# Kernel tuning notes

Measured on AMD Instinct MI355X. Metric: run time of the kernel, lower is better.

Reference implementation:

```python
import jax, jax.numpy as jnp
import numpy as np

WS = (5, 8, 8)   # window_size (Wz, Wh, Ww)
SS = (2, 4, 4)   # shift_size  (Sz, Sh, Sw)
EPS = 1e-5


def _rel_pos_index(ws):
    Wz, Wh, Ww = ws
    coords = np.stack(np.meshgrid(np.arange(Wz), np.arange(Wh), np.arange(Ww), indexing='ij'))
    cf = coords.reshape(3, -1)                      # (3, N)
    rel = cf[:, :, None] - cf[:, None, :]           # (3, N, N)
    rel = rel.transpose(1, 2, 0).astype(np.int64)   # (N, N, 3)
    rel[..., 0] += Wz - 1
    rel[..., 1] += Wh - 1
    rel[..., 2] += Ww - 1
    rel[..., 0] *= (2 * Wh - 1) * (2 * Ww - 1)
    rel[..., 1] *= (2 * Ww - 1)
    return rel.sum(-1)                              # (N, N)


def _shift_mask(Z, H, W, ws, ss):
    Wz, Wh, Ww = ws
    Sz, Sh, Sw = ss
    img = np.zeros((Z, H, W), dtype=np.float32)
    cnt = 0
    for zs in (slice(0, -Wz), slice(-Wz, -Sz), slice(-Sz, None)):
        for hs in (slice(0, -Wh), slice(-Wh, -Sh), slice(-Sh, None)):
            for wl in (slice(0, -Ww), slice(-Ww, -Sw), slice(-Sw, None)):
                img[zs, hs, wl] = cnt
                cnt += 1
    mw = img.reshape(Z // Wz, Wz, H // Wh, Wh, W // Ww, Ww)
    mw = mw.transpose(0, 2, 4, 1, 3, 5).reshape(-1, Wz * Wh * Ww)  # (nW, N)
    diff = mw[:, None, :] - mw[:, :, None]                          # (nW, N, N)
    return np.where(diff != 0, np.float32(-100.0), np.float32(0.0))


def _layernorm(x, g, b):
    mu = jnp.mean(x, axis=-1, keepdims=True)
    var = jnp.var(x, axis=-1, keepdims=True)
    return (x - mu) * jax.lax.rsqrt(var + EPS) * g + b


def setup_inputs() -> dict:
    key = jax.random.key(0)
    ks = jax.random.split(key, 6)
    B, C, Z, H, W = 2, 192, 10, 48, 48
    nH = 6
    hidden = 4 * C
    tbl = (2 * WS[0] - 1) * (2 * WS[1] - 1) * (2 * WS[2] - 1)
    return {
        'x': jax.random.normal(ks[0], (B, C, Z, H, W), jnp.float32),
        'norm1_g': jnp.ones((C,), jnp.float32),
        'norm1_b': jnp.zeros((C,), jnp.float32),
        'qkv_w': jax.random.normal(ks[1], (3 * C, C), jnp.float32) * 0.02,
        'qkv_b': jnp.zeros((3 * C,), jnp.float32),
        'proj_w': jax.random.normal(ks[2], (C, C), jnp.float32) * 0.02,
        'proj_b': jnp.zeros((C,), jnp.float32),
        'rpb_table': jax.random.normal(ks[3], (tbl, nH), jnp.float32) * 0.02,
        'norm2_g': jnp.ones((C,), jnp.float32),
        'norm2_b': jnp.zeros((C,), jnp.float32),
        'fc1_w': jax.random.normal(ks[4], (hidden, C), jnp.float32) * 0.02,
        'fc1_b': jnp.zeros((hidden,), jnp.float32),
        'fc2_w': jax.random.normal(ks[5], (C, hidden), jnp.float32) * 0.02,
        'fc2_b': jnp.zeros((C,), jnp.float32),
    }


def reference(x, norm1_g, norm1_b, qkv_w, qkv_b, proj_w, proj_b, rpb_table,
              norm2_g, norm2_b, fc1_w, fc1_b, fc2_w, fc2_b):
    B, C, Z, H, W = x.shape
    Wz, Wh, Ww = WS
    Sz, Sh, Sw = SS
    nH = rpb_table.shape[1]
    hd = C // nH
    N = Wz * Wh * Ww
    scale = hd ** -0.5

    h = jnp.transpose(x, (0, 2, 3, 4, 1))            # (B,Z,H,W,C) channels-last
    shortcut = h
    h = _layernorm(h, norm1_g, norm1_b)
    # cyclic shift
    h = jnp.roll(h, shift=(-Sz, -Sh, -Sw), axis=(1, 2, 3))
    # window partition -> (BW, N, C)
    win = h.reshape(B, Z // Wz, Wz, H // Wh, Wh, W // Ww, Ww, C)
    win = win.transpose(0, 1, 3, 5, 2, 4, 6, 7).reshape(-1, N, C)
    BW = win.shape[0]

    qkv = win @ qkv_w.T + qkv_b                      # (BW, N, 3C)
    qkv = qkv.reshape(BW, N, 3, nH, hd)
    q = jnp.transpose(qkv[:, :, 0], (0, 2, 1, 3)) * scale   # (BW,nH,N,hd)
    k = jnp.transpose(qkv[:, :, 1], (0, 2, 1, 3))
    v = jnp.transpose(qkv[:, :, 2], (0, 2, 1, 3))

    attn = jnp.einsum('bhnd,bhmd->bhnm', q, k)       # (BW,nH,N,N)
    idx = _rel_pos_index(WS)                          # static (N,N)
    bias = rpb_table[idx.reshape(-1)].reshape(N, N, nH)
    attn = attn + jnp.transpose(bias, (2, 0, 1))[None]

    mask = jnp.asarray(_shift_mask(Z, H, W, WS, SS)) # (nW,N,N), static
    nW = mask.shape[0]
    attn = attn.reshape(B, nW, nH, N, N) + mask[None, :, None]
    attn = jax.nn.softmax(attn.reshape(BW, nH, N, N), axis=-1)

    out = jnp.einsum('bhnm,bhmd->bhnd', attn, v)     # (BW,nH,N,hd)
    out = jnp.transpose(out, (0, 2, 1, 3)).reshape(BW, N, C)
    out = out @ proj_w.T + proj_b

    # window reverse -> (B,Z,H,W,C)
    out = out.reshape(B, Z // Wz, H // Wh, W // Ww, Wz, Wh, Ww, C)
    out = out.transpose(0, 1, 4, 2, 5, 3, 6, 7).reshape(B, Z, H, W, C)
    out = jnp.roll(out, shift=(Sz, Sh, Sw), axis=(1, 2, 3))

    h = shortcut + out
    h2 = _layernorm(h, norm2_g, norm2_b)
    h2 = jax.nn.gelu(h2 @ fc1_w.T + fc1_b, approximate=False)
    h2 = h2 @ fc2_w.T + fc2_b
    h = h + h2
    return jnp.transpose(h, (0, 4, 1, 2, 3))          # back to (B,C,Z,H,W)
```

## Files before the change

### kernel.cpp

```cpp
#include <hip/hip_runtime.h>
#include <hip/hip_bf16.h>

typedef __hip_bfloat16 bf16;
typedef __attribute__((ext_vector_type(4))) float f32x4;
typedef __attribute__((ext_vector_type(8))) short bf16x8;
typedef __attribute__((ext_vector_type(4))) short bf16x4;
typedef __attribute__((ext_vector_type(4))) int i32x4;

#define DEVINL __device__ __forceinline__

constexpr int SPB = 23040;
constexpr int TOK = 46080;
constexpr int NWT = 320;
constexpr int NHEAD = 6;
constexpr int HD = 32;
constexpr int HID = 768;
constexpr int TBL = 2025;
constexpr float SCALE = 0.17677669529663687f;

DEVINL float b2f(bf16 v) { return __bfloat162float(v); }
DEVINL float bflo(unsigned u) { unsigned w = u << 16; return __builtin_bit_cast(float, w); }

DEVINL unsigned cvtpk(float a, float b) {
  unsigned r;
  asm("v_cvt_pk_bf16_f32 %0, %1, %2" : "=v"(r) : "v"(a), "v"(b));
  return r;
}

DEVINL f32x4 mfma16(bf16x4 a, bf16x4 b, f32x4 c) {
#if __has_builtin(__builtin_amdgcn_mfma_f32_16x16x16bf16_1k)
  return __builtin_amdgcn_mfma_f32_16x16x16bf16_1k(a, b, c, 0, 0, 0);
#elif __has_builtin(__builtin_amdgcn_mfma_f32_16x16x16_bf16)
  return __builtin_amdgcn_mfma_f32_16x16x16_bf16(a, b, c, 0, 0, 0);
#else
  f32x4 d;
  asm volatile("v_mfma_f32_16x16x16_bf16 %0, %1, %2, %3\n\ts_nop 7\n\ts_nop 7"
               : "=v"(d) : "v"(a), "v"(b), "v"(c));
  return d;
#endif
}

DEVINL void gload16(const bf16* g, bf16* l) {
  __builtin_amdgcn_global_load_lds(
      (const __attribute__((address_space(1))) void*)g,
      (__attribute__((address_space(3))) void*)l, 16, 0, 0);
}

__global__ void k_flag(const unsigned* __restrict__ g1, int* __restrict__ flag) {
  if (threadIdx.x == 0) flag[0] = (g1[0] == 0x3F800000u) ? 1 : 0;
}

struct CvtArgs {
  const void* src[13];
  bf16* dst[13];
  int n[13];
};

__global__ __launch_bounds__(256) void k_cvt(CvtArgs a, const int* __restrict__ flag) {
  int bi = blockIdx.y;
  int n = a.n[bi];
  bool f32m = flag[0] != 0;
  const float* sf = (const float*)a.src[bi];
  const bf16* sh = (const bf16*)a.src[bi];
  bf16* d = a.dst[bi];
  if (f32m) {
    for (int i = blockIdx.x * 256 + threadIdx.x; i < n; i += gridDim.x * 256)
      d[i] = __float2bfloat16(sf[i]);
  } else {
    for (int i = blockIdx.x * 256 + threadIdx.x; i < n; i += gridDim.x * 256)
      d[i] = sh[i];
  }
}

__global__ __launch_bounds__(256) void k_ln1win(
    const void* __restrict__ xv, const bf16* __restrict__ g, const bf16* __restrict__ be,
    const int* __restrict__ flag, float* __restrict__ hbuf, bf16* __restrict__ win) {
  __shared__ float tile[192][64];
  __shared__ float red[2][4][64];
  __shared__ float stat[2][64];
  int t = threadIdx.x;
  int p = t & 63, q = t >> 6;
  int base = blockIdx.x * 64;
  int b = base / SPB, s0 = base % SPB;
  bool f32m = flag[0] != 0;
  float sum = 0.f, sq = 0.f;
  if (f32m) {
    const float* x = (const float*)xv;
    for (int c = q; c < 192; c += 4) {
      float v = x[(long)(b * 192 + c) * SPB + s0 + p];
      tile[c][p] = v; sum += v; sq += v * v;
    }
  } else {
    const bf16* x = (const bf16*)xv;
    for (int c = q; c < 192; c += 4) {
      float v = b2f(x[(long)(b * 192 + c) * SPB + s0 + p]);
      tile[c][p] = v; sum += v; sq += v * v;
    }
  }
  red[0][q][p] = sum; red[1][q][p] = sq;
  __syncthreads();
  if (t < 64) {
    float s1 = red[0][0][t] + red[0][1][t] + red[0][2][t] + red[0][3][t];
    float s2 = red[1][0][t] + red[1][1][t] + red[1][2][t] + red[1][3][t];
    float mu = s1 * (1.f / 192.f);
    float var = s2 * (1.f / 192.f) - mu * mu;
    stat[0][t] = mu;
    stat[1][t] = rsqrtf(var + 1e-5f);
  }
  __syncthreads();
  int p2 = t >> 2, quad = t & 3;
  int spos = s0 + p2;
  int z = spos / 2304, rm = spos % 2304;
  int hh = rm / 48, ww = rm % 48;
  int zr = z - 2; if (zr < 0) zr += 10;
  int hr = hh - 4; if (hr < 0) hr += 48;
  int wr = ww - 4; if (wr < 0) wr += 48;
  int zw = zr / 5, zi = zr - zw * 5;
  int hw = hr >> 3, hi = hr & 7;
  int wv = wr >> 3, wi = wr & 7;
  int wb = ((b * 2 + zw) * 6 + hw) * 6 + wv;
  int n = (zi * 8 + hi) * 8 + wi;
  float mu = stat[0][p2], rs = stat[1][p2];
  long hb = (long)(b * SPB + spos) * 192;
  long wbse = (long)(wb * NWT + n) * 192;
  for (int c = quad * 48; c < quad * 48 + 48; ++c) {
    float v = tile[c][p2];
    hbuf[hb + c] = v;
    win[wbse + c] = __float2bfloat16((v - mu) * rs * b2f(g[c]) + b2f(be[c]));
  }
}

template <int EPI, int NN>
__global__ __launch_bounds__(256, 5) void k_gemm(
    const bf16* __restrict__ A, const bf16* __restrict__ Wt, const bf16* __restrict__ bias,
    int K, bf16* __restrict__ out0, float* __restrict__ hbuf, void* __restrict__ outb,
    const int* __restrict__ flag) {
  __shared__ __align__(16) char smem[24576];
  bf16* As = (bf16*)smem;
  bf16* Bs = (bf16*)(smem + 16384);

  int t = threadIdx.x;
  constexpr int NBLK = 360 * NN;
  int wg = (blockIdx.x & 7) * (NBLK / 8) + (blockIdx.x >> 3);
  int m0 = (wg / NN) * 128, n0 = (wg % NN) * 64;
  int wave = t >> 6, lane = t & 63;
  int lr = lane & 15, lg = lane >> 4;
  int wbase = t & ~63;
  f32x4 acc[2][4];
#pragma unroll
  for (int a = 0; a < 2; ++a)
#pragma unroll
    for (int bb2 = 0; bb2 < 4; ++bb2) acc[a][bb2] = (f32x4){0.f, 0.f, 0.f, 0.f};

  for (int kc = 0; kc < K; kc += 64) {
#pragma unroll
    for (int it = 0; it < 4; ++it) {
      int s = it * 256 + t;
      int r = s >> 3, c = s & 7;
      int cg = c ^ (r & 7);
      gload16(&A[(long)(m0 + r) * K + kc + cg * 8], As + (it * 256 + wbase) * 8);
    }
#pragma unroll
    for (int it = 0; it < 2; ++it) {
      int s = it * 256 + t;
      int r = s >> 3, c = s & 7;
      int cg = c ^ (r & 7);
      gload16(&Wt[(long)(n0 + r) * K + kc + cg * 8], Bs + (it * 256 + wbase) * 8);
    }
    __syncthreads();
#pragma unroll
    for (int ks = 0; ks < 2; ++ks) {
      int ra = wave * 32 + lr;
      bf16x8 a0 = *(const bf16x8*)(As + ra * 64 + (((ks * 4 + lg) ^ (ra & 7)) * 8));
      bf16x8 a1 = *(const bf16x8*)(As + (ra + 16) * 64 + (((ks * 4 + lg) ^ ((ra + 16) & 7)) * 8));
#pragma unroll
      for (int nn = 0; nn < 4; ++nn) {
        int rb = nn * 16 + lr;
        bf16x8 bfr = *(const bf16x8*)(Bs + rb * 64 + (((ks * 4 + lg) ^ (rb & 7)) * 8));
        acc[0][nn] = __builtin_amdgcn_mfma_f32_16x16x32_bf16(a0, bfr, acc[0][nn], 0, 0, 0);
        acc[1][nn] = __builtin_amdgcn_mfma_f32_16x16x32_bf16(a1, bfr, acc[1][nn], 0, 0, 0);
      }
    }
    __syncthreads();
  }

  if constexpr (EPI == 0) {
    bf16* Ct = (bf16*)smem;
#pragma unroll
    for (int nn = 0; nn < 4; ++nn) {
      int f = n0 + nn * 16 + lr;
      float bv = b2f(bias[f]);
      float sc = (f < 192) ? SCALE : 1.f;
#pragma unroll
      for (int mi = 0; mi < 2; ++mi)
#pragma unroll
        for (int r = 0; r < 4; ++r) {
          int rl = wave * 32 + mi * 16 + lg * 4 + r;
          Ct[rl * 72 + nn * 16 + lr] = __float2bfloat16((acc[mi][nn][r] + bv) * sc);
        }
    }
    __syncthreads();
#pragma unroll
    for (int it = 0; it < 4; ++it) {
      int fi = it * 256 + t;
      int row = fi >> 3, c8 = (fi & 7) * 8;
      int f0 = n0 + c8;
      int plane = f0 >> 5, d0 = f0 & 31;
      long dst = ((long)plane * TOK + m0 + row) * 32 + d0;
      *(i32x4*)&out0[dst] = *(const i32x4*)&Ct[row * 72 + c8];
    }
  } else if constexpr (EPI == 1) {
    float* Cf = (float*)smem;
#pragma unroll
    for (int half = 0; half < 2; ++half) {
      if ((wave >> 1) == half) {
#pragma unroll
        for (int nn = 0; nn < 4; ++nn) {
          int c = n0 + nn * 16 + lr;
          float bv = b2f(bias[c]);
#pragma unroll
          for (int mi = 0; mi < 2; ++mi)
#pragma unroll
            for (int r = 0; r < 4; ++r) {
              int rl = wave * 32 + mi * 16 + lg * 4 + r - half * 64;
              Cf[rl * 68 + nn * 16 + lr] = acc[mi][nn][r] + bv;
            }
        }
      }
      __syncthreads();
#pragma unroll
      for (int it = 0; it < 4; ++it) {
        int fi = it * 256 + t;
        int row = fi >> 4, c4 = (fi & 15) * 4;
        int grow = m0 + half * 64 + row;
        int wb = grow / NWT, i = grow % NWT;
        int b = wb / 72, wIdx = wb % 72;
        int zw = wIdx / 36, hw = (wIdx % 36) / 6, wv = wIdx % 6;
        int zi = i >> 6, hi = (i >> 3) & 7, wi = i & 7;
        int zf = zw * 5 + zi + 2; if (zf >= 10) zf -= 10;
        int hf = hw * 8 + hi + 4; if (hf >= 48) hf -= 48;
        int wf = wv * 8 + wi + 4; if (wf >= 48) wf -= 48;
        long hb = (long)(b * SPB + zf * 2304 + hf * 48 + wf) * 192 + n0 + c4;
        f32x4 cur = *(f32x4*)&hbuf[hb];
        cur += *(const f32x4*)&Cf[row * 68 + c4];
        *(f32x4*)&hbuf[hb] = cur;
      }
      __syncthreads();
    }
  } else if constexpr (EPI == 2) {
    bf16* Ct = (bf16*)smem;
#pragma unroll
    for (int nn = 0; nn < 4; ++nn) {
      int f = n0 + nn * 16 + lr;
      float bv = b2f(bias[f]);
#pragma unroll
      for (int mi = 0; mi < 2; ++mi)
#pragma unroll
        for (int r = 0; r < 4; ++r) {
          int rl = wave * 32 + mi * 16 + lg * 4 + r;
          float v = acc[mi][nn][r] + bv;
          v = 0.5f * v * (1.f + erff(v * 0.70710678118654752f));
          Ct[rl * 72 + nn * 16 + lr] = __float2bfloat16(v);
        }
    }
    __syncthreads();
#pragma unroll
    for (int it = 0; it < 4; ++it) {
      int fi = it * 256 + t;
      int row = fi >> 3, c8 = (fi & 7) * 8;
      long dst = (long)(m0 + row) * HID + n0 + c8;
      *(i32x4*)&out0[dst] = *(const i32x4*)&Ct[row * 72 + c8];
    }
  } else {
    float* eld = (float*)smem;
    int b = m0 / SPB, sbase = m0 % SPB;
    bool f32m = flag[0] != 0;
#pragma unroll
    for (int half = 0; half < 2; ++half) {
      if ((wave >> 1) == half) {
#pragma unroll
        for (int nn = 0; nn < 4; ++nn) {
          int c = n0 + nn * 16 + lr;
          float bv = b2f(bias[c]);
#pragma unroll
          for (int mi = 0; mi < 2; ++mi)
#pragma unroll
            for (int r = 0; r < 4; ++r) {
              int rl = wave * 32 + mi * 16 + lg * 4 + r;
              int row = m0 + rl;
              float v = acc[mi][nn][r] + bv + hbuf[(long)row * 192 + c];
              eld[(rl - half * 64) * 65 + nn * 16 + lr] = v;
            }
        }
      }
      __syncthreads();
      int cl = t >> 2, sq = t & 3;
      long ob = (long)(b * 192 + n0 + cl) * SPB + sbase + half * 64;
      if (f32m) {
        float* ob32 = (float*)outb;
#pragma unroll
        for (int k2 = 0; k2 < 16; ++k2) {
          int sl = sq * 16 + k2;
          ob32[ob + sl] = eld[sl * 65 + cl];
        }
      } else {
        bf16* ob16 = (bf16*)outb;
#pragma unroll
        for (int k2 = 0; k2 < 16; ++k2) {
          int sl = sq * 16 + k2;
          ob16[ob + sl] = __float2bfloat16(eld[sl * 65 + cl]);
        }
      }
      __syncthreads();
    }
  }
}

__global__ __launch_bounds__(256, 3) void k_attn_mfma(
    const bf16* __restrict__ qkv, const bf16* __restrict__ rpb, bf16* __restrict__ o) {
  __shared__ __align__(16) bf16 KlA[320 * 32];
  __shared__ __align__(16) bf16 QlA[320 * 32];
  __shared__ __align__(16) bf16 Vt[32][328];
  __shared__ unsigned short bias_l[2032];
  __shared__ unsigned short info[320];

  int t = threadIdx.x;
  int blk = blockIdx.x;
  int head = blk % NHEAD, wb = blk / NHEAD;
  const bf16* qp = qkv + ((long)head * TOK + wb * NWT) * HD;
  const bf16* kp = qkv + ((long)(6 + head) * TOK + wb * NWT) * HD;
  const bf16* vp = qkv + ((long)(12 + head) * TOK + wb * NWT) * HD;
  int wIdx = wb % 72;
  int wz = wIdx / 36, hw = (wIdx % 36) / 6, wv = wIdx % 6;
  int wbase = t & ~63;

#pragma unroll
  for (int it = 0; it < 5; ++it) {
    int s = it * 256 + t;
    int row = s >> 2, c = s & 3;
    int cg = c ^ (row & 3);
    gload16(&kp[row * 32 + cg * 8], KlA + (it * 256 + wbase) * 8);
    gload16(&qp[row * 32 + cg * 8], QlA + (it * 256 + wbase) * 8);
  }
#pragma unroll
  for (int it = 0; it < 3; ++it) {
    int idx = t + 256 * it;
    if (idx < 640) {
      int kp2 = idx % 160, c8 = idx / 160;
      i32x4 va = *(const i32x4*)&vp[(kp2 * 2) * HD + c8 * 8];
      i32x4 vb = *(const i32x4*)&vp[(kp2 * 2 + 1) * HD + c8 * 8];
#pragma unroll
      for (int e = 0; e < 8; ++e) {
        unsigned lo = ((unsigned)va[e >> 1] >> ((e & 1) * 16)) & 0xffffu;
        unsigned hi = ((unsigned)vb[e >> 1] >> ((e & 1) * 16)) & 0xffffu;
        *(unsigned*)&Vt[c8 * 8 + e][kp2 * 2] = lo | (hi << 16);
      }
    }
  }
  for (int idx = t; idx < TBL; idx += 256)
    bias_l[idx] = ((const unsigned short*)rpb)[idx * NHEAD + head];
  for (int idx = t; idx < NWT; idx += 256) {
    int zi = idx >> 6, hi2 = (idx >> 3) & 7, wi = idx & 7;
    int zr = wz * 5 + zi, hr = hw * 8 + hi2, wr = wv * 8 + wi;
    int rid = (zr < 5 ? 0 : (zr < 8 ? 9 : 18)) + (hr < 40 ? 0 : (hr < 44 ? 3 : 6)) +
              (wr < 40 ? 0 : (wr < 44 ? 1 : 2));
    info[idx] = (unsigned short)(((zi * 225 + hi2 * 15 + wi) << 5) | rid);
  }
  __syncthreads();

  int wave = t >> 6, lane = t & 63;
  int lr = lane & 15, lg = lane >> 4;

  unsigned cj01[20], cj23[20];
#pragma unroll
  for (int tt = 0; tt < 20; ++tt) {
    int k0 = tt * 16 + lg * 4;
    cj01[tt] = *(const unsigned*)&info[k0];
    cj23[tt] = *(const unsigned*)&info[k0 + 2];
  }

  int csw = (lg ^ (lr & 3)) * 8;

  for (int qi = 0; qi < 5; ++qi) {
    int qbl = qi * 64 + wave * 16;
    bf16x8 qf = *(const bf16x8*)(QlA + (qbl + lr) * 32 + csw);
    f32x4 sc[20];
#pragma unroll
    for (int tt = 0; tt < 20; ++tt) {
      bf16x8 kf = *(const bf16x8*)(KlA + (tt * 16 + lr) * 32 + csw);
      sc[tt] = __builtin_amdgcn_mfma_f32_16x16x32_bf16(kf, qf, (f32x4){0.f, 0.f, 0.f, 0.f}, 0, 0, 0);
    }
    unsigned ciq = info[qbl + lr];
    int ci1012 = (int)(ciq >> 5) + 1012;
    float mxv = -1e30f;
#pragma unroll
    for (int tt = 0; tt < 20; ++tt) {
      unsigned w0 = cj01[tt], w1 = cj23[tt];
      unsigned kin0 = w0 & 0xffffu, kin1 = w0 >> 16;
      unsigned kin2 = w1 & 0xffffu, kin3 = w1 >> 16;
      float s0 = sc[tt][0] + bflo((unsigned)bias_l[ci1012 - (int)(kin0 >> 5)]);
      float s1 = sc[tt][1] + bflo((unsigned)bias_l[ci1012 - (int)(kin1 >> 5)]);
      float s2 = sc[tt][2] + bflo((unsigned)bias_l[ci1012 - (int)(kin2 >> 5)]);
      float s3 = sc[tt][3] + bflo((unsigned)bias_l[ci1012 - (int)(kin3 >> 5)]);
      if ((kin0 ^ ciq) & 31u) s0 -= 100.f;
      if ((kin1 ^ ciq) & 31u) s1 -= 100.f;
      if ((kin2 ^ ciq) & 31u) s2 -= 100.f;
      if ((kin3 ^ ciq) & 31u) s3 -= 100.f;
      sc[tt][0] = s0; sc[tt][1] = s1; sc[tt][2] = s2; sc[tt][3] = s3;
      mxv = fmaxf(mxv, fmaxf(fmaxf(s0, s1), fmaxf(s2, s3)));
    }
    mxv = fmaxf(mxv, __shfl_xor(mxv, 16));
    mxv = fmaxf(mxv, __shfl_xor(mxv, 32));
    float sum = 0.f;
#pragma unroll
    for (int tt = 0; tt < 20; ++tt) {
      float p0 = __expf(sc[tt][0] - mxv);
      float p1 = __expf(sc[tt][1] - mxv);
      float p2 = __expf(sc[tt][2] - mxv);
      float p3 = __expf(sc[tt][3] - mxv);
      sc[tt][0] = p0; sc[tt][1] = p1; sc[tt][2] = p2; sc[tt][3] = p3;
      sum += (p0 + p1) + (p2 + p3);
    }
    sum += __shfl_xor(sum, 16);
    sum += __shfl_xor(sum, 32);
    float rl = 1.f / sum;

    f32x4 oacc0 = {0.f, 0.f, 0.f, 0.f}, oacc1 = {0.f, 0.f, 0.f, 0.f};
#pragma unroll
    for (int tt = 0; tt < 20; ++tt) {
      unsigned pk0 = cvtpk(sc[tt][0], sc[tt][1]);
      unsigned pk1 = cvtpk(sc[tt][2], sc[tt][3]);
      union { unsigned u[2]; bf16x4 v; } pu;
      pu.u[0] = pk0; pu.u[1] = pk1;
      bf16x4 v0 = *(const bf16x4*)&Vt[lr][tt * 16 + lg * 4];
      bf16x4 v1 = *(const bf16x4*)&Vt[16 + lr][tt * 16 + lg * 4];
      oacc0 = mfma16(pu.v, v0, oacc0);
      oacc1 = mfma16(pu.v, v1, oacc1);
    }
    int rli = __builtin_bit_cast(int, rl);
    float rl4[4];
#pragma unroll
    for (int r = 0; r < 4; ++r)
      rl4[r] = __builtin_bit_cast(float, __builtin_amdgcn_ds_bpermute((lg * 4 + r) * 4, rli));
#pragma unroll
    for (int r = 0; r < 4; ++r) {
      bf16* pr = o + ((long)(wb * NWT) + qbl + lg * 4 + r) * 192 + head * 32;
      pr[lr] = __float2bfloat16(oacc0[r] * rl4[r]);
      pr[16 + lr] = __float2bfloat16(oacc1[r] * rl4[r]);
    }
  }
}

__global__ __launch_bounds__(192) void k_ln2(
    const float* __restrict__ h, const bf16* __restrict__ g, const bf16* __restrict__ be,
    bf16* __restrict__ o) {
  __shared__ float r1[3], r2[3];
  int t = threadIdx.x;
  long row = blockIdx.x;
  float vv = h[row * 192 + t];
  float s1 = vv, s2 = vv * vv;
#pragma unroll
  for (int off = 32; off > 0; off >>= 1) {
    s1 += __shfl_down(s1, off);
    s2 += __shfl_down(s2, off);
  }
  if ((t & 63) == 0) { r1[t >> 6] = s1; r2[t >> 6] = s2; }
  __syncthreads();
  float sum = r1[0] + r1[1] + r1[2];
  float sq = r2[0] + r2[1] + r2[2];
  float mu = sum * (1.f / 192.f);
  float rs = rsqrtf(sq * (1.f / 192.f) - mu * mu + 1e-5f);
  o[row * 192 + t] = __float2bfloat16((vv - mu) * rs * b2f(g[t]) + b2f(be[t]));
}

extern "C" void kernel_launch(void* const* d_in, const int* in_sizes, int n_in,
                              void* d_out, int out_size, void* d_ws, size_t ws_size,
                              hipStream_t stream) {
  (void)in_sizes; (void)n_in; (void)out_size; (void)ws_size;

  char* pp = (char*)d_ws;
  float* hbuf = (float*)pp;        pp += (size_t)TOK * 192 * 4;
  bf16* qkv   = (bf16*)pp;         pp += (size_t)3 * TOK * 192 * 2;
  bf16* win   = (bf16*)pp;         pp += (size_t)TOK * 192 * 2;
  bf16* fc1o  = (bf16*)pp;         pp += (size_t)TOK * HID * 2;
  int*  flag  = (int*)pp;          pp += 64;

  const int din_idx[13] = {1, 2, 3, 4, 5, 6, 7, 8, 9, 10, 11, 12, 13};
  const int sizes[13]   = {192, 192, 110592, 576, 36864, 192, 12150, 192, 192,
                           147456, 768, 147456, 192};
  bf16* canon[13];
  for (int ii = 0; ii < 13; ++ii) {
    canon[ii] = (bf16*)pp;
    size_t bytes = ((size_t)sizes[ii] * 2 + 63) & ~(size_t)63;
    pp += bytes;
  }
  bf16* n1g  = canon[0];
  bf16* n1b  = canon[1];
  bf16* qkvw = canon[2];
  bf16* qkvb = canon[3];
  bf16* projw= canon[4];
  bf16* projb= canon[5];
  bf16* rpb  = canon[6];
  bf16* n2g  = canon[7];
  bf16* n2b  = canon[8];
  bf16* fc1w = canon[9];
  bf16* fc1b = canon[10];
  bf16* fc2w = canon[11];
  bf16* fc2b = canon[12];

  CvtArgs ca;
  for (int ii = 0; ii < 13; ++ii) {
    ca.src[ii] = d_in[din_idx[ii]];
    ca.dst[ii] = canon[ii];
    ca.n[ii] = sizes[ii];
  }

  k_flag<<<1, 64, 0, stream>>>((const unsigned*)d_in[1], flag);
  k_cvt<<<dim3(64, 13), 256, 0, stream>>>(ca, flag);
  k_ln1win<<<TOK / 64, 256, 0, stream>>>(d_in[0], n1g, n1b, flag, hbuf, win);
  k_gemm<0, 9><<<360 * 9, 256, 0, stream>>>(win, qkvw, qkvb, 192, qkv, nullptr, nullptr, flag);
  k_attn_mfma<<<864, 256, 0, stream>>>(qkv, rpb, win);
  k_gemm<1, 3><<<360 * 3, 256, 0, stream>>>(win, projw, projb, 192, nullptr, hbuf, nullptr, flag);
  k_ln2<<<TOK, 192, 0, stream>>>(hbuf, n2g, n2b, win);
  k_gemm<2, 12><<<360 * 12, 256, 0, stream>>>(win, fc1w, fc1b, 192, fc1o, nullptr, nullptr, flag);
  k_gemm<3, 3><<<360 * 3, 256, 0, stream>>>(fc1o, fc2w, fc2b, 768, nullptr, hbuf, d_out, flag);
}
```

Before: 269.4 us.

## Precompute dense bias+mask tables per head and window class, shrink attention LDS

Adds a kernel that builds dense 320x320 bf16 tables of relative-position bias combined with the shift mask. There is one table for each of the 6 heads and 8 window boundary classes, stored in the fc1 output scratch buffer. The attention kernel then reads bias values directly from global/L2 instead of gathering from an LDS copy of the table and evaluating mask region ids. Q fragments are held in registers, and the Q buffer is reused for the transposed V, which cuts LDS use and may allow higher occupancy. The cost is an extra launch that writes about 9.8 MB, plus per-row global bias reads in the softmax loop.

```diff
diff --git a/kernel.cpp b/kernel.cpp
--- a/kernel.cpp
+++ b/kernel.cpp
@@ -20,6 +20,7 @@
 
 DEVINL float b2f(bf16 v) { return __bfloat162float(v); }
 DEVINL float bflo(unsigned u) { unsigned w = u << 16; return __builtin_bit_cast(float, w); }
+DEVINL float bfhi(unsigned u) { unsigned w = u & 0xffff0000u; return __builtin_bit_cast(float, w); }
 
 DEVINL unsigned cvtpk(float a, float b) {
   unsigned r;
@@ -70,6 +71,24 @@
     for (int i = blockIdx.x * 256 + threadIdx.x; i < n; i += gridDim.x * 256)
       d[i] = sh[i];
   }
+}
+
+__global__ __launch_bounds__(320) void k_bias(const bf16* __restrict__ rpb,
+                                              bf16* __restrict__ bm) {
+  int i = blockIdx.x;
+  int hc = blockIdx.y;
+  int cls = hc & 7, head = hc >> 3;
+  int j = threadIdx.x;
+  int zi = i >> 6, hi = (i >> 3) & 7, wi = i & 7;
+  int zj = j >> 6, hj = (j >> 3) & 7, wj = j & 7;
+  int idx = (zi - zj) * 225 + (hi - hj) * 15 + (wi - wj) + 1012;
+  float b = b2f(rpb[idx * NHEAD + head]);
+  int ri = ((cls & 4) ? (zi < 3 ? 9 : 18) : 0) + ((cls & 2) ? (hi < 4 ? 3 : 6) : 0) +
+           ((cls & 1) ? (wi < 4 ? 1 : 2) : 0);
+  int rj = ((cls & 4) ? (zj < 3 ? 9 : 18) : 0) + ((cls & 2) ? (hj < 4 ? 3 : 6) : 0) +
+           ((cls & 1) ? (wj < 4 ? 1 : 2) : 0);
+  if (ri != rj) b -= 100.f;
+  bm[((long)hc * 320 + i) * 320 + j] = __float2bfloat16(b);
 }
 
 __global__ __launch_bounds__(256) void k_ln1win(
@@ -317,12 +336,9 @@
 }
 
 __global__ __launch_bounds__(256, 3) void k_attn_mfma(
-    const bf16* __restrict__ qkv, const bf16* __restrict__ rpb, bf16* __restrict__ o) {
+    const bf16* __restrict__ qkv, const bf16* __restrict__ biasM, bf16* __restrict__ o) {
   __shared__ __align__(16) bf16 KlA[320 * 32];
-  __shared__ __align__(16) bf16 QlA[320 * 32];
-  __shared__ __align__(16) bf16 Vt[32][328];
-  __shared__ unsigned short bias_l[2032];
-  __shared__ unsigned short info[320];
+  __shared__ __align__(16) bf16 OvA[32 * 328];
 
   int t = threadIdx.x;
   int blk = blockIdx.x;
@@ -331,7 +347,9 @@
   const bf16* kp = qkv + ((long)(6 + head) * TOK + wb * NWT) * HD;
   const bf16* vp = qkv + ((long)(12 + head) * TOK + wb * NWT) * HD;
   int wIdx = wb % 72;
-  int wz = wIdx / 36, hw = (wIdx % 36) / 6, wv = wIdx % 6;
+  int cls = ((wIdx >= 36) ? 4 : 0) | ((((wIdx % 36) / 6) == 5) ? 2 : 0) |
+            (((wIdx % 6) == 5) ? 1 : 0);
+  const bf16* bmh = biasM + (long)(head * 8 + cls) * 320 * 320;
   int wbase = t & ~63;
 
 #pragma unroll
@@ -340,72 +358,64 @@
     int row = s >> 2, c = s & 3;
     int cg = c ^ (row & 3);
     gload16(&kp[row * 32 + cg * 8], KlA + (it * 256 + wbase) * 8);
-    gload16(&qp[row * 32 + cg * 8], QlA + (it * 256 + wbase) * 8);
-  }
+    gload16(&qp[row * 32 + cg * 8], OvA + (it * 256 + wbase) * 8);
+  }
+  i32x4 va[3], vb[3];
 #pragma unroll
   for (int it = 0; it < 3; ++it) {
     int idx = t + 256 * it;
     if (idx < 640) {
       int kp2 = idx % 160, c8 = idx / 160;
-      i32x4 va = *(const i32x4*)&vp[(kp2 * 2) * HD + c8 * 8];
-      i32x4 vb = *(const i32x4*)&vp[(kp2 * 2 + 1) * HD + c8 * 8];
-#pragma unroll
-      for (int e = 0; e < 8; ++e) {
-        unsigned lo = ((unsigned)va[e >> 1] >> ((e & 1) * 16)) & 0xffffu;
-        unsigned hi = ((unsigned)vb[e >> 1] >> ((e & 1) * 16)) & 0xffffu;
-        *(unsigned*)&Vt[c8 * 8 + e][kp2 * 2] = lo | (hi << 16);
-      }
-    }
-  }
-  for (int idx = t; idx < TBL; idx += 256)
-    bias_l[idx] = ((const unsigned short*)rpb)[idx * NHEAD + head];
-  for (int idx = t; idx < NWT; idx += 256) {
-    int zi = idx >> 6, hi2 = (idx >> 3) & 7, wi = idx & 7;
-    int zr = wz * 5 + zi, hr = hw * 8 + hi2, wr = wv * 8 + wi;
-    int rid = (zr < 5 ? 0 : (zr < 8 ? 9 : 18)) + (hr < 40 ? 0 : (hr < 44 ? 3 : 6)) +
-              (wr < 40 ? 0 : (wr < 44 ? 1 : 2));
-    info[idx] = (unsigned short)(((zi * 225 + hi2 * 15 + wi) << 5) | rid);
+      va[it] = *(const i32x4*)&vp[(kp2 * 2) * HD + c8 * 8];
+      vb[it] = *(const i32x4*)&vp[(kp2 * 2 + 1) * HD + c8 * 8];
+    }
   }
   __syncthreads();
 
   int wave = t >> 6, lane = t & 63;
   int lr = lane & 15, lg = lane >> 4;
-
-  unsigned cj01[20], cj23[20];
-#pragma unroll
-  for (int tt = 0; tt < 20; ++tt) {
-    int k0 = tt * 16 + lg * 4;
-    cj01[tt] = *(const unsigned*)&info[k0];
-    cj23[tt] = *(const unsigned*)&info[k0 + 2];
-  }
-
   int csw = (lg ^ (lr & 3)) * 8;
+
+  bf16x8 qreg[5];
+#pragma unroll
+  for (int qi = 0; qi < 5; ++qi)
+    qreg[qi] = *(const bf16x8*)(OvA + (qi * 64 + wave * 16 + lr) * 32 + csw);
+  __syncthreads();
+
+#pragma unroll
+  for (int it = 0; it < 3; ++it) {
+    int idx = t + 256 * it;
+    if (idx < 640) {
+      int kp2 = idx % 160, c8 = idx / 160;
+#pragma unroll
+      for (int e = 0; e < 8; ++e) {
+        unsigned lo = ((unsigned)va[it][e >> 1] >> ((e & 1) * 16)) & 0xffffu;
+        unsigned hi = ((unsigned)vb[it][e >> 1] >> ((e & 1) * 16)) & 0xffffu;
+        *(unsigned*)&OvA[(c8 * 8 + e) * 328 + kp2 * 2] = lo | (hi << 16);
+      }
+    }
+  }
+  __syncthreads();
 
   for (int qi = 0; qi < 5; ++qi) {
     int qbl = qi * 64 + wave * 16;
-    bf16x8 qf = *(const bf16x8*)(QlA + (qbl + lr) * 32 + csw);
+    bf16x8 qf = qreg[qi];
+    const bf16* bmr = bmh + (long)(qbl + lr) * 320;
     f32x4 sc[20];
 #pragma unroll
     for (int tt = 0; tt < 20; ++tt) {
       bf16x8 kf = *(const bf16x8*)(KlA + (tt * 16 + lr) * 32 + csw);
       sc[tt] = __builtin_amdgcn_mfma_f32_16x16x32_bf16(kf, qf, (f32x4){0.f, 0.f, 0.f, 0.f}, 0, 0, 0);
     }
-    unsigned ciq = info[qbl + lr];
-    int ci1012 = (int)(ciq >> 5) + 1012;
     float mxv = -1e30f;
 #pragma unroll
     for (int tt = 0; tt < 20; ++tt) {
-      unsigned w0 = cj01[tt], w1 = cj23[tt];
-      unsigned kin0 = w0 & 0xffffu, kin1 = w0 >> 16;
-      unsigned kin2 = w1 & 0xffffu, kin3 = w1 >> 16;
-      float s0 = sc[tt][0] + bflo((unsigned)bias_l[ci1012 - (int)(kin0 >> 5)]);
-      float s1 = sc[tt][1] + bflo((unsigned)bias_l[ci1012 - (int)(kin1 >> 5)]);
-      float s2 = sc[tt][2] + bflo((unsigned)bias_l[ci1012 - (int)(kin2 >> 5)]);
-      float s3 = sc[tt][3] + bflo((unsigned)bias_l[ci1012 - (int)(kin3 >> 5)]);
-      if ((kin0 ^ ciq) & 31u) s0 -= 100.f;
-      if ((kin1 ^ ciq) & 31u) s1 -= 100.f;
-      if ((kin2 ^ ciq) & 31u) s2 -= 100.f;
-      if ((kin3 ^ ciq) & 31u) s3 -= 100.f;
+      union { bf16x4 v; unsigned u[2]; } bu;
+      bu.v = *(const bf16x4*)&bmr[tt * 16 + lg * 4];
+      float s0 = sc[tt][0] + bflo(bu.u[0]);
+      float s1 = sc[tt][1] + bfhi(bu.u[0]);
+      float s2 = sc[tt][2] + bflo(bu.u[1]);
+      float s3 = sc[tt][3] + bfhi(bu.u[1]);
       sc[tt][0] = s0; sc[tt][1] = s1; sc[tt][2] = s2; sc[tt][3] = s3;
       mxv = fmaxf(mxv, fmaxf(fmaxf(s0, s1), fmaxf(s2, s3)));
     }
@@ -432,8 +442,8 @@
       unsigned pk1 = cvtpk(sc[tt][2], sc[tt][3]);
       union { unsigned u[2]; bf16x4 v; } pu;
       pu.u[0] = pk0; pu.u[1] = pk1;
-      bf16x4 v0 = *(const bf16x4*)&Vt[lr][tt * 16 + lg * 4];
-      bf16x4 v1 = *(const bf16x4*)&Vt[16 + lr][tt * 16 + lg * 4];
+      bf16x4 v0 = *(const bf16x4*)&OvA[lr * 328 + tt * 16 + lg * 4];
+      bf16x4 v1 = *(const bf16x4*)&OvA[(16 + lr) * 328 + tt * 16 + lg * 4];
       oacc0 = mfma16(pu.v, v0, oacc0);
       oacc1 = mfma16(pu.v, v1, oacc1);
     }
@@ -484,6 +494,8 @@
   bf16* win   = (bf16*)pp;         pp += (size_t)TOK * 192 * 2;
   bf16* fc1o  = (bf16*)pp;         pp += (size_t)TOK * HID * 2;
   int*  flag  = (int*)pp;          pp += 64;
+
+  bf16* biasM = fc1o;
 
   const int din_idx[13] = {1, 2, 3, 4, 5, 6, 7, 8, 9, 10, 11, 12, 13};
   const int sizes[13]   = {192, 192, 110592, 576, 36864, 192, 12150, 192, 192,
@@ -517,9 +529,10 @@
 
   k_flag<<<1, 64, 0, stream>>>((const unsigned*)d_in[1], flag);
   k_cvt<<<dim3(64, 13), 256, 0, stream>>>(ca, flag);
+  k_bias<<<dim3(320, 48), 320, 0, stream>>>(rpb, biasM);
   k_ln1win<<<TOK / 64, 256, 0, stream>>>(d_in[0], n1g, n1b, flag, hbuf, win);
   k_gemm<0, 9><<<360 * 9, 256, 0, stream>>>(win, qkvw, qkvb, 192, qkv, nullptr, nullptr, flag);
-  k_attn_mfma<<<864, 256, 0, stream>>>(qkv, rpb, win);
+  k_attn_mfma<<<864, 256, 0, stream>>>(qkv, biasM, win);
   k_gemm<1, 3><<<360 * 3, 256, 0, stream>>>(win, projw, projb, 192, nullptr, hbuf, nullptr, flag);
   k_ln2<<<TOK, 192, 0, stream>>>(hbuf, n2g, n2b, win);
   k_gemm<2, 12><<<360 * 12, 256, 0, stream>>>(win, fc1w, fc1b, 192, fc1o, nullptr, nullptr, flag);
```

New measurement: 357.4 us. 1.33x slower.
